# Kernel tuning notes

Measured on AMD Instinct MI355X. Metric: run time of the kernel, lower is better.

The kernel has to match this reference:

```python
import jax, jax.numpy as jnp
import numpy as np

F = 128   # flattened observation features
H = 64    # MLP/LSTM hidden size (hardcoded in module)
A = 15    # number of discrete actions
T = 128   # rollout length (timesteps)
B = 2048  # number of parallel envs (batch)


def setup_inputs() -> dict:
    key = jax.random.key(0)
    ks = jax.random.split(key, 12)
    n = lambda k, sh, s=1.0: jax.random.normal(k, sh, jnp.float32) * s
    return {
        "x": n(ks[0], (T * B, F)),
        "done": (jax.random.uniform(ks[1], (T * B,)) < 0.05).astype(jnp.float32),
        "h0": n(ks[2], (1, B, H)),
        "c0": n(ks[3], (1, B, H)),
        # MLP encoder params (Linear stores y = x @ W + b here, W: [in, out])
        "W1": n(ks[4], (F, H), 0.1), "b1": jnp.zeros((H,), jnp.float32),
        "W2": n(ks[5], (H, H), 0.1), "b2": jnp.zeros((H,), jnp.float32),
        # LSTM params, PyTorch layout: weight_ih [4H, H_in], gate order i,f,g,o
        "Wih": n(ks[6], (4 * H, H), 0.1), "bih": jnp.zeros((4 * H,), jnp.float32),
        "Whh": n(ks[7], (4 * H, H), 0.1), "bhh": jnp.zeros((4 * H,), jnp.float32),
        # actor / critic heads
        "Wa": n(ks[8], (H, A), 0.01), "ba": jnp.zeros((A,), jnp.float32),
        "Wc": n(ks[9], (H, 1), 1.0), "bc": jnp.zeros((1,), jnp.float32),
    }


def reference(x, done, h0, c0, W1, b1, W2, b2, Wih, bih, Whh, bhh, Wa, ba, Wc, bc):
    Bsz, Hh = h0.shape[1], h0.shape[2]
    # MLP encoder: Linear -> Tanh -> Linear -> Tanh
    y = jnp.tanh(x @ W1 + b1)
    y = jnp.tanh(y @ W2 + b2)                 # [T*B, H]
    y = y.reshape(-1, Bsz, Hh)                # [T, B, H]
    d = done.reshape(-1, Bsz)                 # [T, B]

    def step(carry, td):
        h, c = carry
        yt, dt = td
        m = (1.0 - dt)[:, None]               # done-mask hidden reset
        h = h * m
        c = c * m
        g = yt @ Wih.T + bih + h @ Whh.T + bhh  # [B, 4H]
        i, f, gg, o = jnp.split(g, 4, axis=-1)
        c = jax.nn.sigmoid(f) * c + jax.nn.sigmoid(i) * jnp.tanh(gg)
        h = jax.nn.sigmoid(o) * jnp.tanh(c)
        return (h, c), h

    (hT, cT), outs = jax.lax.scan(step, (h0[0], c0[0]), (y, d))
    z = outs.reshape(-1, Hh)                  # [T*B, H]
    logits = z @ Wa + ba                      # Categorical logits
    vf = z @ Wc + bc
    return logits, vf, hT[None], cT[None]
```

## Files before the change

kernel.cpp:

```cpp
#include <hip/hip_runtime.h>
#include <hip/hip_bf16.h>
#include <stdint.h>

typedef __bf16  bf16x8 __attribute__((ext_vector_type(8)));
typedef short   s16x8  __attribute__((ext_vector_type(8)));
typedef int     i32x4  __attribute__((ext_vector_type(4)));
typedef float   f32x4  __attribute__((ext_vector_type(4)));

union Frag { s16x8 s; bf16x8 b; i32x4 i; };

static __device__ __forceinline__ short f2bf(float f) {
    union { float f; unsigned u; } v; v.f = f;
    unsigned r = (v.u + 0x7FFFu + ((v.u >> 16) & 1u)) >> 16;
    return (short)r;
}
static __device__ __forceinline__ float bf2f(short s) {
    union { unsigned u; float f; } v; v.u = ((unsigned)(unsigned short)s) << 16;
    return v.f;
}
static __device__ __forceinline__ float fast_rcp(float x) { return __builtin_amdgcn_rcpf(x); }
static __device__ __forceinline__ float sigm(float x) { return fast_rcp(1.0f + __expf(-x)); }
static __device__ __forceinline__ float tanh_fast(float x) {
    float e = __expf(-2.0f * x);
    return (1.0f - e) * fast_rcp(1.0f + e);
}
static __device__ __forceinline__ f32x4 mfma16(bf16x8 a, bf16x8 b, f32x4 c) {
    return __builtin_amdgcn_mfma_f32_16x16x32_bf16(a, b, c, 0, 0, 0);
}

#define GLDS(gp, lp) __builtin_amdgcn_global_load_lds( \
    (const __attribute__((address_space(1))) void*)(gp), \
    (__attribute__((address_space(3))) void*)(lp), 16, 0, 0)

#define TT 128
#define BB 2048
#define HH 64
#define FF 128
#define AA 15
#define CH 8
#define LOGITS_OFF 0
#define VF_OFF   3932160
#define HT_OFF   4194304
#define CT_OFF   4325376


__global__ __launch_bounds__(256) void enc_kernel(
    const float* __restrict__ x, const float* __restrict__ W1, const float* __restrict__ b1,
    const float* __restrict__ W2, const float* __restrict__ b2, short* __restrict__ y_sw)
{
    __shared__ short w1t[64][136];
    __shared__ short w2t[64][72];
    __shared__ short c1buf[4][16][72];
    __shared__ short ybuf[4][16][72];

    const int tid  = threadIdx.x;
    const int lane = tid & 63;
    const int w    = tid >> 6;
    const int c    = lane & 15;
    const int q    = lane >> 4;

    for (int i = tid; i < 128*64; i += 256) { int k = i >> 6, n = i & 63; w1t[n][k] = f2bf(W1[i]); }
    for (int i = tid; i < 64*64;  i += 256) { int k = i >> 6, n = i & 63; w2t[n][k] = f2bf(W2[i]); }

    float b1v[4], b2v[4];
#pragma unroll
    for (int ct = 0; ct < 4; ++ct) { b1v[ct] = b1[16*ct + c]; b2v[ct] = b2[16*ct + c]; }
    __syncthreads();

    for (int it = 0; it < 4; ++it) {
        const int wt = it*4096 + blockIdx.x*4 + w;
        const int r0 = wt * 16;
        Frag af[4];
#pragma unroll
        for (int kf = 0; kf < 4; ++kf) {
            const float* xp = x + (size_t)(r0 + c)*FF + 32*kf + 8*q;
            f32x4 x0 = *(const f32x4*)xp;
            f32x4 x1 = *(const f32x4*)(xp + 4);
#pragma unroll
            for (int jj = 0; jj < 4; ++jj) { af[kf].s[jj] = f2bf(x0[jj]); af[kf].s[4+jj] = f2bf(x1[jj]); }
        }
        f32x4 acc[4];
#pragma unroll
        for (int ct = 0; ct < 4; ++ct) acc[ct] = (f32x4){b1v[ct], b1v[ct], b1v[ct], b1v[ct]};
#pragma unroll
        for (int kf = 0; kf < 4; ++kf)
#pragma unroll
            for (int ct = 0; ct < 4; ++ct) {
                Frag bf; bf.s = *(const s16x8*)&w1t[16*ct + c][32*kf + 8*q];
                acc[ct] = mfma16(af[kf].b, bf.b, acc[ct]);
            }
#pragma unroll
        for (int ct = 0; ct < 4; ++ct)
#pragma unroll
            for (int i = 0; i < 4; ++i)
                c1buf[w][4*q + i][16*ct + c] = f2bf(tanh_fast(acc[ct][i]));
        Frag a2[2];
#pragma unroll
        for (int kf = 0; kf < 2; ++kf) a2[kf].s = *(const s16x8*)&c1buf[w][c][32*kf + 8*q];
        f32x4 acc2[4];
#pragma unroll
        for (int ct = 0; ct < 4; ++ct) acc2[ct] = (f32x4){b2v[ct], b2v[ct], b2v[ct], b2v[ct]};
#pragma unroll
        for (int kf = 0; kf < 2; ++kf)
#pragma unroll
            for (int ct = 0; ct < 4; ++ct) {
                Frag bf; bf.s = *(const s16x8*)&w2t[16*ct + c][32*kf + 8*q];
                acc2[ct] = mfma16(a2[kf].b, bf.b, acc2[ct]);
            }
#pragma unroll
        for (int ct = 0; ct < 4; ++ct)
#pragma unroll
            for (int i = 0; i < 4; ++i)
                ybuf[w][4*q + i][16*ct + c] = f2bf(tanh_fast(acc2[ct][i]));
#pragma unroll
        for (int kf = 0; kf < 2; ++kf) {
            s16x8 yv = *(const s16x8*)&ybuf[w][c][32*kf + 8*q];
            *(s16x8*)(y_sw + (size_t)wt*1024 + kf*512 + lane*8) = yv;
        }
    }
}

__global__ __launch_bounds__(512, 1) void scan_kernel(
    const short* __restrict__ y_sw, const float* __restrict__ done,
    const float* __restrict__ h0, const float* __restrict__ c0,
    const float* __restrict__ Wih, const float* __restrict__ bih,
    const float* __restrict__ Whh, const float* __restrict__ bhh,
    const float* __restrict__ Wa, const float* __restrict__ ba,
    const float* __restrict__ Wc, const float* __restrict__ bc,
    float* __restrict__ out_logits, float* __restrict__ out_vf,
    float* __restrict__ hT_out, float* __restrict__ cT_out)
{
    __shared__ short ybuf[2][CH][1024];
    __shared__ float gybuf[2][4][4][256];
    __shared__ float obuf[2][CH][16][16];
    __shared__ short zbuf[2][16][72];
    __shared__ short hbuf[2][16][72];
    __shared__ float dbuf[TT+1][16];

    const int tid  = threadIdx.x;
    const int lane = tid & 63;
    const int w    = tid >> 6;
    const int c    = lane & 15;
    const int q    = lane >> 4;
    const int blk  = blockIdx.x;
    const int b0   = blk * 16;
    const bool crit = (w < 4);
    const int hw   = w - 4;

    Frag  wf[4][2];
    float biasv[4];
    Frag  hwf[2];
    float hbv = 0.f;
    float cst[4];

    if (crit) {
        const int jcol = 16*w + c;
#pragma unroll
        for (int a = 0; a < 4; ++a) {
            const int col = 64*a + jcol;
#pragma unroll
            for (int kf = 0; kf < 2; ++kf) {
                const float* wp = Whh + (size_t)col*HH + 32*kf + 8*q;
                f32x4 w0 = *(const f32x4*)wp;
                f32x4 w1 = *(const f32x4*)(wp + 4);
#pragma unroll
                for (int jj = 0; jj < 4; ++jj) { wf[a][kf].s[jj] = f2bf(w0[jj]); wf[a][kf].s[4+jj] = f2bf(w1[jj]); }
            }
        }
    } else {
        const int jcolh = 16*hw + c;
#pragma unroll
        for (int a = 0; a < 4; ++a) {
            const int col = 64*a + jcolh;
            biasv[a] = bih[col] + bhh[col];
#pragma unroll
            for (int kf = 0; kf < 2; ++kf) {
                const float* wp = Wih + (size_t)col*HH + 32*kf + 8*q;
                f32x4 w0 = *(const f32x4*)wp;
                f32x4 w1 = *(const f32x4*)(wp + 4);
#pragma unroll
                for (int jj = 0; jj < 4; ++jj) { wf[a][kf].s[jj] = f2bf(w0[jj]); wf[a][kf].s[4+jj] = f2bf(w1[jj]); }
            }
        }
#pragma unroll
        for (int kf = 0; kf < 2; ++kf)
#pragma unroll
            for (int jj = 0; jj < 8; ++jj) {
                int k = 32*kf + 8*q + jj;
                hwf[kf].s[jj] = f2bf((c < 15) ? Wa[k*AA + c] : Wc[k]);
            }
        hbv = (c < 15) ? ba[c] : bc[0];
#pragma unroll
        for (int i = 0; i < 2; ++i) {
            int j = hw*2 + i;
            const float* gp = done + (size_t)(16*j + (lane >> 2))*BB + b0 + 4*(lane & 3);
            GLDS(gp, &dbuf[16*j][0]);
        }
#pragma unroll
        for (int i = 0; i < 4; ++i) {
            int idx = hw*4 + i, ss = idx >> 1, half = idx & 1;
            const short* gp = y_sw + ((size_t)ss*128 + blk)*1024 + half*512 + lane*8;
            GLDS(gp, &ybuf[0][ss][half*512]);
        }
        __builtin_amdgcn_s_waitcnt(0x0F70);
    }
    if (tid < 16) dbuf[TT][tid] = 0.0f;
    __syncthreads();

    if (crit) {
        const int jcol = 16*w + c;
#pragma unroll
        for (int i = 0; i < 4; ++i) {
            float d0 = dbuf[0][4*q + i];
            float cv = c0[(size_t)(b0 + 4*q + i)*HH + jcol];
            cst[i] = (d0 != 0.0f) ? 0.0f : cv;
        }
        int mm = tid & 15, j4 = (tid >> 4) & 15;
        float dm = dbuf[0][mm];
        f32x4 hv = *(const f32x4*)(h0 + (size_t)(b0 + mm)*HH + 4*j4);
#pragma unroll
        for (int ii = 0; ii < 4; ++ii)
            hbuf[0][mm][4*j4 + ii] = (dm != 0.0f) ? (short)0 : f2bf(hv[ii]);
    } else {
        Frag yc0, yc1;
        yc0.s = *(const s16x8*)&ybuf[0][0][lane*8];
        yc1.s = *(const s16x8*)&ybuf[0][0][512 + lane*8];
#pragma unroll
        for (int a = 0; a < 4; ++a) {
            f32x4 g = (f32x4){biasv[a], biasv[a], biasv[a], biasv[a]};
            g = mfma16(yc0.b, wf[0+a][0].b, g);
            g = mfma16(yc1.b, wf[a][1].b, g);
            f32x4 gg = (f32x4){biasv[a], biasv[a], biasv[a], biasv[a]};
            gg = mfma16(yc0.b, wf[a][0].b, gg);
            gg = mfma16(yc1.b, wf[a][1].b, gg);
            *(f32x4*)&gybuf[0][hw][a][lane*4] = gg;
        }
    }
    __syncthreads();

    for (int t = 0; t < TT; ++t) {
        if (crit) {
            const int jcol = 16*w + c;
            const int cur = t & 1;
            Frag hf0, hf1;
            hf0.s = *(const s16x8*)&hbuf[cur][c][8*q];
            hf1.s = *(const s16x8*)&hbuf[cur][c][32 + 8*q];
            f32x4 acc[4];
#pragma unroll
            for (int a = 0; a < 4; ++a) acc[a] = *(const f32x4*)&gybuf[cur][w][a][lane*4];
#pragma unroll
            for (int a = 0; a < 4; ++a) {
                acc[a] = mfma16(hf0.b, wf[a][0].b, acc[a]);
                acc[a] = mfma16(hf1.b, wf[a][1].b, acc[a]);
            }
            const f32x4 dn = *(const f32x4*)&dbuf[t+1][4*q];
#pragma unroll
            for (int i = 0; i < 4; ++i) {
                float gi = acc[0][i], gf = acc[1][i], gg = acc[2][i], go = acc[3][i];
                float cn = sigm(gf)*cst[i] + sigm(gi)*tanh_fast(gg);
                float h  = sigm(go)*tanh_fast(cn);
                short zb = f2bf(h);
                zbuf[cur][4*q + i][jcol] = zb;
                const bool d = (dn[i] != 0.0f);
                cst[i] = d ? 0.0f : cn;
                hbuf[cur ^ 1][4*q + i][jcol] = d ? (short)0 : zb;
            }
        } else {
            if ((t & 7) == 0 && t < 120) {
                const int k = (t >> 3) + 1;
#pragma unroll
                for (int i = 0; i < 4; ++i) {
                    int idx = hw*4 + i, ss = idx >> 1, half = idx & 1;
                    const short* gp = y_sw + ((size_t)(8*k + ss)*128 + blk)*1024 + half*512 + lane*8;
                    GLDS(gp, &ybuf[k & 1][ss][half*512]);
                }
            }
            if ((t & 7) == 1 && t > 8 && w < 6) {
                const int cc = (t >> 3) - 1;
                const int idx = (w - 4)*64 + lane;
                const int s = idx >> 4, r = idx & 15;
                const size_t row = (size_t)(8*cc + s)*BB + b0 + r;
                const float* ob = &obuf[cc & 1][s][r][0];
                float* lp = out_logits + row*AA;
#pragma unroll
                for (int n = 0; n < 15; ++n) lp[n] = ob[n];
                out_vf[row] = ob[15];
            }
            if (t >= 1 && w == 4 + ((t-1) & 3)) {
                const int tp = t - 1;
                Frag zf0, zf1;
                zf0.s = *(const s16x8*)&zbuf[tp & 1][c][8*q];
                zf1.s = *(const s16x8*)&zbuf[tp & 1][c][32 + 8*q];
                f32x4 ha = (f32x4){hbv, hbv, hbv, hbv};
                ha = mfma16(zf0.b, hwf[0].b, ha);
                ha = mfma16(zf1.b, hwf[1].b, ha);
#pragma unroll
                for (int i = 0; i < 4; ++i)
                    obuf[(tp >> 3) & 1][tp & 7][4*q + i][c] = ha[i];
            }
            if (t < TT-1) {
                const int tn = t + 1;
                const int ch = (tn >> 3) & 1, sl = tn & 7;
                Frag yc0, yc1;
                yc0.s = *(const s16x8*)&ybuf[ch][sl][lane*8];
                yc1.s = *(const s16x8*)&ybuf[ch][sl][512 + lane*8];
#pragma unroll
                for (int a = 0; a < 4; ++a) {
                    f32x4 g = (f32x4){biasv[a], biasv[a], biasv[a], biasv[a]};
                    g = mfma16(yc0.b, wf[a][0].b, g);
                    g = mfma16(yc1.b, wf[a][1].b, g);
                    *(f32x4*)&gybuf[tn & 1][hw][a][lane*4] = g;
                }
            }
            if ((t & 7) == 6)
                __builtin_amdgcn_s_waitcnt(0x0F70);
        }
        __syncthreads();
    }

    if (!crit && w == 7) {
        Frag zf0, zf1;
        zf0.s = *(const s16x8*)&zbuf[1][c][8*q];
        zf1.s = *(const s16x8*)&zbuf[1][c][32 + 8*q];
        f32x4 ha = (f32x4){hbv, hbv, hbv, hbv};
        ha = mfma16(zf0.b, hwf[0].b, ha);
        ha = mfma16(zf1.b, hwf[1].b, ha);
#pragma unroll
        for (int i = 0; i < 4; ++i) obuf[1][7][4*q + i][c] = ha[i];
    }
    __syncthreads();
    if (!crit && w < 6) {
        const int idx = (w - 4)*64 + lane;
        const int s = idx >> 4, r = idx & 15;
        const size_t row = (size_t)(120 + s)*BB + b0 + r;
        const float* ob = &obuf[1][s][r][0];
        float* lp = out_logits + row*AA;
#pragma unroll
        for (int n = 0; n < 15; ++n) lp[n] = ob[n];
        out_vf[row] = ob[15];
    }
    if (crit) {
        const int jcol = 16*w + c;
        int mm = tid & 15, j4 = (tid >> 4) & 15;
        f32x4 hv;
#pragma unroll
        for (int ii = 0; ii < 4; ++ii) hv[ii] = bf2f(zbuf[1][mm][4*j4 + ii]);
        *(f32x4*)(hT_out + (size_t)(b0 + mm)*HH + 4*j4) = hv;
#pragma unroll
        for (int i = 0; i < 4; ++i) cT_out[(size_t)(b0 + 4*q + i)*HH + jcol] = cst[i];
    }
}

extern "C" void kernel_launch(void* const* d_in, const int* in_sizes, int n_in,
                              void* d_out, int out_size, void* d_ws, size_t ws_size,
                              hipStream_t stream) {
    const float* x    = (const float*)d_in[0];
    const float* done = (const float*)d_in[1];
    const float* h0   = (const float*)d_in[2];
    const float* c0   = (const float*)d_in[3];
    const float* W1   = (const float*)d_in[4];
    const float* b1   = (const float*)d_in[5];
    const float* W2   = (const float*)d_in[6];
    const float* b2   = (const float*)d_in[7];
    const float* Wih  = (const float*)d_in[8];
    const float* bih  = (const float*)d_in[9];
    const float* Whh  = (const float*)d_in[10];
    const float* bhh  = (const float*)d_in[11];
    const float* Wa   = (const float*)d_in[12];
    const float* ba   = (const float*)d_in[13];
    const float* Wc   = (const float*)d_in[14];
    const float* bc   = (const float*)d_in[15];
    float* out = (float*)d_out;

    short* y_sw = (short*)d_ws;

    enc_kernel<<<1024, 256, 0, stream>>>(x, W1, b1, W2, b2, y_sw);
    scan_kernel<<<128, 512, 0, stream>>>(y_sw, done, h0, c0, Wih, bih, Whh, bhh,
                                         Wa, ba, Wc, bc,
                                         out + LOGITS_OFF, out + VF_OFF,
                                         out + HT_OFF, out + CT_OFF);
}
```

Baseline: 317.8 us.

## Split LSTM recurrence across all eight waves and keep input gates in registers

Replaces the producer/consumer split (four waves doing the recurrent MFMA and cell update, four waves precomputing input projections and heads) with a symmetric scheme. Every wave holds both Whh and Wih fragments, computes the recurrent MFMAs redundantly for its column slice, and applies the elementwise cell update to only half of the rows. The next step's input-projection MFMA runs in registers, which removes the gybuf LDS round trip. The head outputs now go straight to global memory instead of being staged through obuf, at the cost of redundant MFMA work, more registers, and scattered narrow stores.

Measured after the change: 346.1 us. 8.9% more time.

```diff
diff --git a/kernel.cpp b/kernel.cpp
--- a/kernel.cpp
+++ b/kernel.cpp
@@ -131,8 +131,6 @@
     float* __restrict__ hT_out, float* __restrict__ cT_out)
 {
     __shared__ short ybuf[2][CH][1024];
-    __shared__ float gybuf[2][4][4][256];
-    __shared__ float obuf[2][CH][16][16];
     __shared__ short zbuf[2][16][72];
     __shared__ short hbuf[2][16][72];
     __shared__ float dbuf[TT+1][16];
@@ -140,185 +138,159 @@
     const int tid  = threadIdx.x;
     const int lane = tid & 63;
     const int w    = tid >> 6;
+    const int wc   = w & 3;
+    const int wh   = w >> 2;
     const int c    = lane & 15;
     const int q    = lane >> 4;
     const int blk  = blockIdx.x;
     const int b0   = blk * 16;
-    const bool crit = (w < 4);
-    const int hw   = w - 4;
+    const int jcol = 16*wc + c;
 
     Frag  wf[4][2];
+    Frag  wfi[4][2];
+    Frag  hwf[2];
     float biasv[4];
-    Frag  hwf[2];
-    float hbv = 0.f;
-    float cst[4];
-
-    if (crit) {
-        const int jcol = 16*w + c;
-#pragma unroll
-        for (int a = 0; a < 4; ++a) {
-            const int col = 64*a + jcol;
-#pragma unroll
-            for (int kf = 0; kf < 2; ++kf) {
-                const float* wp = Whh + (size_t)col*HH + 32*kf + 8*q;
-                f32x4 w0 = *(const f32x4*)wp;
-                f32x4 w1 = *(const f32x4*)(wp + 4);
-#pragma unroll
-                for (int jj = 0; jj < 4; ++jj) { wf[a][kf].s[jj] = f2bf(w0[jj]); wf[a][kf].s[4+jj] = f2bf(w1[jj]); }
-            }
-        }
-    } else {
-        const int jcolh = 16*hw + c;
-#pragma unroll
-        for (int a = 0; a < 4; ++a) {
-            const int col = 64*a + jcolh;
-            biasv[a] = bih[col] + bhh[col];
-#pragma unroll
-            for (int kf = 0; kf < 2; ++kf) {
-                const float* wp = Wih + (size_t)col*HH + 32*kf + 8*q;
-                f32x4 w0 = *(const f32x4*)wp;
-                f32x4 w1 = *(const f32x4*)(wp + 4);
-#pragma unroll
-                for (int jj = 0; jj < 4; ++jj) { wf[a][kf].s[jj] = f2bf(w0[jj]); wf[a][kf].s[4+jj] = f2bf(w1[jj]); }
-            }
-        }
-#pragma unroll
-        for (int kf = 0; kf < 2; ++kf)
-#pragma unroll
-            for (int jj = 0; jj < 8; ++jj) {
-                int k = 32*kf + 8*q + jj;
-                hwf[kf].s[jj] = f2bf((c < 15) ? Wa[k*AA + c] : Wc[k]);
-            }
-        hbv = (c < 15) ? ba[c] : bc[0];
-#pragma unroll
-        for (int i = 0; i < 2; ++i) {
-            int j = hw*2 + i;
-            const float* gp = done + (size_t)(16*j + (lane >> 2))*BB + b0 + 4*(lane & 3);
-            GLDS(gp, &dbuf[16*j][0]);
-        }
-#pragma unroll
-        for (int i = 0; i < 4; ++i) {
-            int idx = hw*4 + i, ss = idx >> 1, half = idx & 1;
-            const short* gp = y_sw + ((size_t)ss*128 + blk)*1024 + half*512 + lane*8;
-            GLDS(gp, &ybuf[0][ss][half*512]);
-        }
-        __builtin_amdgcn_s_waitcnt(0x0F70);
+    float hbv;
+    float cst0, cst1;
+
+#pragma unroll
+    for (int a = 0; a < 4; ++a) {
+        const int col = 64*a + jcol;
+        biasv[a] = bih[col] + bhh[col];
+#pragma unroll
+        for (int kf = 0; kf < 2; ++kf) {
+            const float* wp = Whh + (size_t)col*HH + 32*kf + 8*q;
+            f32x4 w0 = *(const f32x4*)wp;
+            f32x4 w1 = *(const f32x4*)(wp + 4);
+#pragma unroll
+            for (int jj = 0; jj < 4; ++jj) { wf[a][kf].s[jj] = f2bf(w0[jj]); wf[a][kf].s[4+jj] = f2bf(w1[jj]); }
+            const float* vp = Wih + (size_t)col*HH + 32*kf + 8*q;
+            f32x4 v0 = *(const f32x4*)vp;
+            f32x4 v1 = *(const f32x4*)(vp + 4);
+#pragma unroll
+            for (int jj = 0; jj < 4; ++jj) { wfi[a][kf].s[jj] = f2bf(v0[jj]); wfi[a][kf].s[4+jj] = f2bf(v1[jj]); }
+        }
+    }
+#pragma unroll
+    for (int kf = 0; kf < 2; ++kf)
+#pragma unroll
+        for (int jj = 0; jj < 8; ++jj) {
+            int k = 32*kf + 8*q + jj;
+            hwf[kf].s[jj] = f2bf((c < 15) ? Wa[k*AA + c] : Wc[k]);
+        }
+    hbv = (c < 15) ? ba[c] : bc[0];
+
+    {
+        const float* gp = done + (size_t)(16*w + (lane >> 2))*BB + b0 + 4*(lane & 3);
+        GLDS(gp, &dbuf[16*w][0]);
+    }
+#pragma unroll
+    for (int half = 0; half < 2; ++half) {
+        const short* gp = y_sw + ((size_t)w*128 + blk)*1024 + half*512 + lane*8;
+        GLDS(gp, &ybuf[0][w][half*512]);
     }
     if (tid < 16) dbuf[TT][tid] = 0.0f;
+    __builtin_amdgcn_s_waitcnt(0x0F70);
     __syncthreads();
 
-    if (crit) {
-        const int jcol = 16*w + c;
-#pragma unroll
-        for (int i = 0; i < 4; ++i) {
-            float d0 = dbuf[0][4*q + i];
-            float cv = c0[(size_t)(b0 + 4*q + i)*HH + jcol];
-            cst[i] = (d0 != 0.0f) ? 0.0f : cv;
-        }
-        int mm = tid & 15, j4 = (tid >> 4) & 15;
+    {
+        float d0 = dbuf[0][4*q + 2*wh + 0];
+        float d1 = dbuf[0][4*q + 2*wh + 1];
+        float cv0 = c0[(size_t)(b0 + 4*q + 2*wh + 0)*HH + jcol];
+        float cv1 = c0[(size_t)(b0 + 4*q + 2*wh + 1)*HH + jcol];
+        cst0 = (d0 != 0.0f) ? 0.0f : cv0;
+        cst1 = (d1 != 0.0f) ? 0.0f : cv1;
+    }
+    if (tid < 256) {
+        int mm = tid & 15, j4 = tid >> 4;
         float dm = dbuf[0][mm];
         f32x4 hv = *(const f32x4*)(h0 + (size_t)(b0 + mm)*HH + 4*j4);
 #pragma unroll
         for (int ii = 0; ii < 4; ++ii)
             hbuf[0][mm][4*j4 + ii] = (dm != 0.0f) ? (short)0 : f2bf(hv[ii]);
-    } else {
+    }
+    f32x4 gyr[4];
+    {
         Frag yc0, yc1;
         yc0.s = *(const s16x8*)&ybuf[0][0][lane*8];
         yc1.s = *(const s16x8*)&ybuf[0][0][512 + lane*8];
 #pragma unroll
         for (int a = 0; a < 4; ++a) {
             f32x4 g = (f32x4){biasv[a], biasv[a], biasv[a], biasv[a]};
-            g = mfma16(yc0.b, wf[0+a][0].b, g);
-            g = mfma16(yc1.b, wf[a][1].b, g);
-            f32x4 gg = (f32x4){biasv[a], biasv[a], biasv[a], biasv[a]};
-            gg = mfma16(yc0.b, wf[a][0].b, gg);
-            gg = mfma16(yc1.b, wf[a][1].b, gg);
-            *(f32x4*)&gybuf[0][hw][a][lane*4] = gg;
+            g = mfma16(yc0.b, wfi[a][0].b, g);
+            g = mfma16(yc1.b, wfi[a][1].b, g);
+            gyr[a] = g;
         }
     }
     __syncthreads();
 
     for (int t = 0; t < TT; ++t) {
-        if (crit) {
-            const int jcol = 16*w + c;
-            const int cur = t & 1;
-            Frag hf0, hf1;
-            hf0.s = *(const s16x8*)&hbuf[cur][c][8*q];
-            hf1.s = *(const s16x8*)&hbuf[cur][c][32 + 8*q];
-            f32x4 acc[4];
-#pragma unroll
-            for (int a = 0; a < 4; ++a) acc[a] = *(const f32x4*)&gybuf[cur][w][a][lane*4];
+        const int cur = t & 1;
+        Frag hf0, hf1;
+        hf0.s = *(const s16x8*)&hbuf[cur][c][8*q];
+        hf1.s = *(const s16x8*)&hbuf[cur][c][32 + 8*q];
+        if ((t & 7) == 0 && t < 120) {
+            const int k = (t >> 3) + 1;
+#pragma unroll
+            for (int half = 0; half < 2; ++half) {
+                const short* gp = y_sw + ((size_t)(8*k + w)*128 + blk)*1024 + half*512 + lane*8;
+                GLDS(gp, &ybuf[k & 1][w][half*512]);
+            }
+        }
+        Frag yc0, yc1;
+        if (t < TT-1) {
+            const int tn = t + 1;
+            yc0.s = *(const s16x8*)&ybuf[(tn >> 3) & 1][tn & 7][lane*8];
+            yc1.s = *(const s16x8*)&ybuf[(tn >> 3) & 1][tn & 7][512 + lane*8];
+        }
+#pragma unroll
+        for (int a = 0; a < 4; ++a) {
+            gyr[a] = mfma16(hf0.b, wf[a][0].b, gyr[a]);
+            gyr[a] = mfma16(hf1.b, wf[a][1].b, gyr[a]);
+        }
+        const float dn0 = dbuf[t+1][4*q + 2*wh + 0];
+        const float dn1 = dbuf[t+1][4*q + 2*wh + 1];
+#define ELEM(CSTV, I, DN) {                                             \
+            float gi = gyr[0][I], gf = gyr[1][I], gg = gyr[2][I], go = gyr[3][I]; \
+            float cn = sigm(gf)*CSTV + sigm(gi)*tanh_fast(gg);          \
+            float hv = sigm(go)*tanh_fast(cn);                          \
+            short zb = f2bf(hv);                                        \
+            zbuf[cur][4*q + I][jcol] = zb;                              \
+            const bool d = ((DN) != 0.0f);                              \
+            CSTV = d ? 0.0f : cn;                                       \
+            hbuf[cur ^ 1][4*q + I][jcol] = d ? (short)0 : zb; }
+        if (wh == 0) { ELEM(cst0, 0, dn0) ELEM(cst1, 1, dn1) }
+        else         { ELEM(cst0, 2, dn0) ELEM(cst1, 3, dn1) }
+#undef ELEM
+        if (t < TT-1) {
 #pragma unroll
             for (int a = 0; a < 4; ++a) {
-                acc[a] = mfma16(hf0.b, wf[a][0].b, acc[a]);
-                acc[a] = mfma16(hf1.b, wf[a][1].b, acc[a]);
-            }
-            const f32x4 dn = *(const f32x4*)&dbuf[t+1][4*q];
+                f32x4 g = (f32x4){biasv[a], biasv[a], biasv[a], biasv[a]};
+                g = mfma16(yc0.b, wfi[a][0].b, g);
+                g = mfma16(yc1.b, wfi[a][1].b, g);
+                gyr[a] = g;
+            }
+        }
+        if ((t & 7) == 6) __builtin_amdgcn_s_waitcnt(0x0F70);
+        if (t >= 1 && w == ((t-1) & 7)) {
+            const int tp = t - 1;
+            Frag zf0, zf1;
+            zf0.s = *(const s16x8*)&zbuf[tp & 1][c][8*q];
+            zf1.s = *(const s16x8*)&zbuf[tp & 1][c][32 + 8*q];
+            f32x4 ha = (f32x4){hbv, hbv, hbv, hbv};
+            ha = mfma16(zf0.b, hwf[0].b, ha);
+            ha = mfma16(zf1.b, hwf[1].b, ha);
 #pragma unroll
             for (int i = 0; i < 4; ++i) {
-                float gi = acc[0][i], gf = acc[1][i], gg = acc[2][i], go = acc[3][i];
-                float cn = sigm(gf)*cst[i] + sigm(gi)*tanh_fast(gg);
-                float h  = sigm(go)*tanh_fast(cn);
-                short zb = f2bf(h);
-                zbuf[cur][4*q + i][jcol] = zb;
-                const bool d = (dn[i] != 0.0f);
-                cst[i] = d ? 0.0f : cn;
-                hbuf[cur ^ 1][4*q + i][jcol] = d ? (short)0 : zb;
-            }
-        } else {
-            if ((t & 7) == 0 && t < 120) {
-                const int k = (t >> 3) + 1;
-#pragma unroll
-                for (int i = 0; i < 4; ++i) {
-                    int idx = hw*4 + i, ss = idx >> 1, half = idx & 1;
-                    const short* gp = y_sw + ((size_t)(8*k + ss)*128 + blk)*1024 + half*512 + lane*8;
-                    GLDS(gp, &ybuf[k & 1][ss][half*512]);
-                }
-            }
-            if ((t & 7) == 1 && t > 8 && w < 6) {
-                const int cc = (t >> 3) - 1;
-                const int idx = (w - 4)*64 + lane;
-                const int s = idx >> 4, r = idx & 15;
-                const size_t row = (size_t)(8*cc + s)*BB + b0 + r;
-                const float* ob = &obuf[cc & 1][s][r][0];
-                float* lp = out_logits + row*AA;
-#pragma unroll
-                for (int n = 0; n < 15; ++n) lp[n] = ob[n];
-                out_vf[row] = ob[15];
-            }
-            if (t >= 1 && w == 4 + ((t-1) & 3)) {
-                const int tp = t - 1;
-                Frag zf0, zf1;
-                zf0.s = *(const s16x8*)&zbuf[tp & 1][c][8*q];
-                zf1.s = *(const s16x8*)&zbuf[tp & 1][c][32 + 8*q];
-                f32x4 ha = (f32x4){hbv, hbv, hbv, hbv};
-                ha = mfma16(zf0.b, hwf[0].b, ha);
-                ha = mfma16(zf1.b, hwf[1].b, ha);
-#pragma unroll
-                for (int i = 0; i < 4; ++i)
-                    obuf[(tp >> 3) & 1][tp & 7][4*q + i][c] = ha[i];
-            }
-            if (t < TT-1) {
-                const int tn = t + 1;
-                const int ch = (tn >> 3) & 1, sl = tn & 7;
-                Frag yc0, yc1;
-                yc0.s = *(const s16x8*)&ybuf[ch][sl][lane*8];
-                yc1.s = *(const s16x8*)&ybuf[ch][sl][512 + lane*8];
-#pragma unroll
-                for (int a = 0; a < 4; ++a) {
-                    f32x4 g = (f32x4){biasv[a], biasv[a], biasv[a], biasv[a]};
-                    g = mfma16(yc0.b, wf[a][0].b, g);
-                    g = mfma16(yc1.b, wf[a][1].b, g);
-                    *(f32x4*)&gybuf[tn & 1][hw][a][lane*4] = g;
-                }
-            }
-            if ((t & 7) == 6)
-                __builtin_amdgcn_s_waitcnt(0x0F70);
+                const size_t row = (size_t)tp*BB + b0 + 4*q + i;
+                if (c < 15) out_logits[row*AA + c] = ha[i];
+                else        out_vf[row] = ha[i];
+            }
         }
         __syncthreads();
     }
 
-    if (!crit && w == 7) {
+    if (w == 7) {
         Frag zf0, zf1;
         zf0.s = *(const s16x8*)&zbuf[1][c][8*q];
         zf1.s = *(const s16x8*)&zbuf[1][c][32 + 8*q];
@@ -326,29 +298,21 @@
         ha = mfma16(zf0.b, hwf[0].b, ha);
         ha = mfma16(zf1.b, hwf[1].b, ha);
 #pragma unroll
-        for (int i = 0; i < 4; ++i) obuf[1][7][4*q + i][c] = ha[i];
-    }
-    __syncthreads();
-    if (!crit && w < 6) {
-        const int idx = (w - 4)*64 + lane;
-        const int s = idx >> 4, r = idx & 15;
-        const size_t row = (size_t)(120 + s)*BB + b0 + r;
-        const float* ob = &obuf[1][s][r][0];
-        float* lp = out_logits + row*AA;
-#pragma unroll
-        for (int n = 0; n < 15; ++n) lp[n] = ob[n];
-        out_vf[row] = ob[15];
-    }
-    if (crit) {
-        const int jcol = 16*w + c;
-        int mm = tid & 15, j4 = (tid >> 4) & 15;
+        for (int i = 0; i < 4; ++i) {
+            const size_t row = (size_t)127*BB + b0 + 4*q + i;
+            if (c < 15) out_logits[row*AA + c] = ha[i];
+            else        out_vf[row] = ha[i];
+        }
+    }
+    if (tid < 256) {
+        int mm = tid & 15, j4 = tid >> 4;
         f32x4 hv;
 #pragma unroll
         for (int ii = 0; ii < 4; ++ii) hv[ii] = bf2f(zbuf[1][mm][4*j4 + ii]);
         *(f32x4*)(hT_out + (size_t)(b0 + mm)*HH + 4*j4) = hv;
-#pragma unroll
-        for (int i = 0; i < 4; ++i) cT_out[(size_t)(b0 + 4*q + i)*HH + jcol] = cst[i];
-    }
+    }
+    cT_out[(size_t)(b0 + 4*q + 2*wh + 0)*HH + jcol] = cst0;
+    cT_out[(size_t)(b0 + 4*q + 2*wh + 1)*HH + jcol] = cst1;
 }
 
 extern "C" void kernel_launch(void* const* d_in, const int* in_sizes, int n_in,
```
